# Kernel optimization log

Hardware: AMD Instinct MI355X
Metric: run time of the kernel (lower is better)

Reference implementation:

```python
import jax, jax.numpy as jnp
import numpy as np

N = 100000      # nodes
E = 1600000     # edges
G = 1024        # graphs in batch
NF = 9          # atom features (OGB AtomEncoder)
V = 128         # vocab per atom feature
H = 128         # hidden_dim
L = 3           # num_graph_layers
OUT = 10        # output_dim
BN_EPS = 1e-5


def setup_inputs() -> dict:
    key = jax.random.key(0)
    ks = jax.random.split(key, 12)
    x = jax.random.randint(ks[0], (N, NF), 0, V, dtype=jnp.int32)
    edge_index = jax.random.randint(ks[1], (2, E), 0, N, dtype=jnp.int32)
    batch = jnp.sort(jax.random.randint(ks[2], (N,), 0, G, dtype=jnp.int32))
    emb = jax.random.normal(ks[3], (NF, V, H), dtype=jnp.float32) * 0.05
    Ws = jax.random.normal(ks[4], (L, H, H), dtype=jnp.float32) * (1.0 / np.sqrt(H))
    bs = jnp.zeros((L, H), dtype=jnp.float32)
    gamma = jnp.ones((L - 1, H), dtype=jnp.float32)
    beta = jnp.zeros((L - 1, H), dtype=jnp.float32)
    run_mean = jax.random.normal(ks[5], (L - 1, H), dtype=jnp.float32) * 0.1
    run_var = jax.random.uniform(ks[6], (L - 1, H), minval=0.5, maxval=1.5, dtype=jnp.float32)
    W_clf = jax.random.normal(ks[7], (H, OUT), dtype=jnp.float32) * (1.0 / np.sqrt(H))
    b_clf = jnp.zeros((OUT,), dtype=jnp.float32)
    return {"x": x, "edge_index": edge_index, "batch": batch, "emb": emb,
            "Ws": Ws, "bs": bs, "gamma": gamma, "beta": beta,
            "run_mean": run_mean, "run_var": run_var,
            "W_clf": W_clf, "b_clf": b_clf}


def reference(x, edge_index, batch, emb, Ws, bs, gamma, beta, run_mean, run_var, W_clf, b_clf):
    # Eval-mode forward: dropout = identity, BatchNorm uses running stats.
    src, dst = edge_index[0], edge_index[1]
    # GCN symmetric normalization with self-loops: deg = 1 + in-degree
    deg = jax.ops.segment_sum(jnp.ones((E,), jnp.float32), dst, num_segments=N) + 1.0
    dinv = jax.lax.rsqrt(deg)                 # [N]
    norm_e = dinv[src] * dinv[dst]            # [E] edge coefficient
    norm_self = dinv * dinv                   # [N] self-loop coefficient

    # AtomEncoder: sum of per-feature embedding lookups -> [N, H]
    h = emb[jnp.arange(NF)[None, :], x].sum(axis=1)

    for i in range(L):
        hw = h @ Ws[i]                                                       # [N, H]
        h = (jax.ops.segment_sum(hw[src] * norm_e[:, None], dst, num_segments=N)
             + hw * norm_self[:, None] + bs[i])                              # GCNConv
        if i < L - 1:
            h = (h - run_mean[i]) * (gamma[i] * jax.lax.rsqrt(run_var[i] + BN_EPS)) + beta[i]
            h = jax.nn.relu(h)

    # global mean pool over graphs
    counts = jax.ops.segment_sum(jnp.ones((N,), jnp.float32), batch, num_segments=G)
    pooled = jax.ops.segment_sum(h, batch, num_segments=G) / jnp.maximum(counts, 1.0)[:, None]
    return pooled @ W_clf + b_clf             # [G, OUT]
```

## Files before the change

### kernel.cpp

```cpp
#include <hip/hip_runtime.h>
#include <hip/hip_bf16.h>
#include <hip/hip_fp16.h>

#define NN 100000
#define EE 1600000
#define GG 1024
#define NF 9
#define VV 128
#define HH 128
#define LL 3
#define OUTD 10
#define BN_EPS 1e-5f
#define NBUCK 196
#define BCAP 12288
#define CHUNK 4096
#define NSPLIT 391
#define NENC 3125
#define NB128 782

typedef __attribute__((ext_vector_type(8))) short short8;
typedef __attribute__((ext_vector_type(4))) float f32x4;

__device__ inline unsigned short f2bf(float x) {
    unsigned u = __float_as_uint(x);
    unsigned r = (u + 0x7fffu + ((u >> 16) & 1u)) >> 16;
    return (unsigned short)r;
}
__device__ inline float bf2f(unsigned short b) { return __uint_as_float(((unsigned)b) << 16); }

__device__ inline void mix8(float a[8], const uint4& r, float nm) {
    asm("v_fma_mix_f32 %0, %8, %12, %0 op_sel:[0,0,0] op_sel_hi:[1,0,0]\n\t"
        "v_fma_mix_f32 %1, %8, %12, %1 op_sel:[1,0,0] op_sel_hi:[1,0,0]\n\t"
        "v_fma_mix_f32 %2, %9, %12, %2 op_sel:[0,0,0] op_sel_hi:[1,0,0]\n\t"
        "v_fma_mix_f32 %3, %9, %12, %3 op_sel:[1,0,0] op_sel_hi:[1,0,0]\n\t"
        "v_fma_mix_f32 %4, %10, %12, %4 op_sel:[0,0,0] op_sel_hi:[1,0,0]\n\t"
        "v_fma_mix_f32 %5, %10, %12, %5 op_sel:[1,0,0] op_sel_hi:[1,0,0]\n\t"
        "v_fma_mix_f32 %6, %11, %12, %6 op_sel:[0,0,0] op_sel_hi:[1,0,0]\n\t"
        "v_fma_mix_f32 %7, %11, %12, %7 op_sel:[1,0,0] op_sel_hi:[1,0,0]"
        : "+v"(a[0]), "+v"(a[1]), "+v"(a[2]), "+v"(a[3]),
          "+v"(a[4]), "+v"(a[5]), "+v"(a[6]), "+v"(a[7])
        : "v"(r.x), "v"(r.y), "v"(r.z), "v"(r.w), "v"(nm));
}

__global__ __launch_bounds__(256) void wprep_kernel(const float* __restrict__ Ws,
        const float* __restrict__ Wc, const float* __restrict__ b2,
        unsigned short* __restrict__ WThi, unsigned short* __restrict__ WTlo,
        unsigned short* __restrict__ WcThi, unsigned short* __restrict__ WcTlo,
        float* __restrict__ bb2, int* __restrict__ bcur, float* __restrict__ pooled) {
    int id = blockIdx.x * 256 + threadIdx.x;
    if (id < LL * HH * HH) {
        int layer = id >> 14;
        int rem = id & (HH * HH - 1);
        int k = rem >> 7, n = rem & 127;
        float w = Ws[id];
        unsigned short hi = f2bf(w);
        float lo = w - bf2f(hi);
        WThi[(size_t)layer * HH * HH + n * HH + k] = hi;
        WTlo[(size_t)layer * HH * HH + n * HH + k] = f2bf(lo);
    }
    int tid = threadIdx.x;
    if (blockIdx.x == 0) {
        const float* W2 = Ws + (size_t)2 * HH * HH;
        for (int i = tid; i < 16 * HH; i += 256) {
            int n = i >> 7, k = i & 127;
            float s = 0.f;
            if (n < OUTD) {
                for (int j = 0; j < HH; ++j)
                    s += W2[k * HH + j] * Wc[j * OUTD + n];
            }
            unsigned short hi = f2bf(s);
            WcThi[i] = hi;
            WcTlo[i] = f2bf(s - bf2f(hi));
        }
        if (tid < OUTD) {
            float s = 0.f;
            for (int c = 0; c < HH; ++c) s += b2[c] * Wc[c * OUTD + tid];
            bb2[tid] = s;
        }
    } else if (blockIdx.x == 1) {
        bcur[tid] = 0;
    } else if (blockIdx.x >= 2 && blockIdx.x < 66) {
        pooled[(blockIdx.x - 2) * 256 + tid] = 0.f;
    }
}

__global__ __launch_bounds__(256) void split_enc_kernel(
        const int* __restrict__ src, const int* __restrict__ dst,
        int* __restrict__ bcur, int* __restrict__ bucket_edges,
        const int* __restrict__ x, const float* __restrict__ emb,
        const unsigned short* __restrict__ WThi, const unsigned short* __restrict__ WTlo,
        __half* __restrict__ hw_out) {
    __shared__ __align__(16) char smem_raw[25600];
    int tid = threadIdx.x;
    if (blockIdx.x < NSPLIT) {
        int* lcnt  = (int*)smem_raw;
        int* loff  = lcnt + 256;
        int* lcur  = loff + 256;
        int* gbase = lcur + 256;
        int* sh    = gbase + 256;
        int* stage = sh + 256;
        unsigned char* stageb = (unsigned char*)(stage + CHUNK);
        int cs = blockIdx.x * CHUNK;
        int n = min(CHUNK, EE - cs);
        lcnt[tid] = 0;
        __syncthreads();
        for (int i = tid; i < n; i += 256)
            atomicAdd(&lcnt[dst[cs + i] >> 9], 1);
        __syncthreads();
        int val = lcnt[tid];
        sh[tid] = val; __syncthreads();
        for (int d = 1; d < 256; d <<= 1) {
            int t = (tid >= d) ? sh[tid - d] : 0;
            __syncthreads();
            sh[tid] += t;
            __syncthreads();
        }
        loff[tid] = sh[tid] - val;
        lcur[tid] = sh[tid] - val;
        __syncthreads();
        for (int i = tid; i < n; i += 256) {
            int d = dst[cs + i], s = src[cs + i];
            int b = d >> 9;
            int p = atomicAdd(&lcur[b], 1);
            stage[p] = (s << 9) | (d & 511);
            stageb[p] = (unsigned char)b;
        }
        if (val > 0) gbase[tid] = atomicAdd(&bcur[tid], val);
        __syncthreads();
        for (int i = tid; i < n; i += 256) {
            int b = stageb[i];
            bucket_edges[(size_t)b * BCAP + gbase[b] + (i - loff[b])] = stage[i];
        }
    } else {
        unsigned short (*lh)[136] = (unsigned short(*)[136])smem_raw;
        unsigned short (*ll)[136] = (unsigned short(*)[136])(smem_raw + 32 * 136 * 2);
        int nloc = tid >> 3;
        int seg = tid & 7;
        int nodebase = (blockIdx.x - NSPLIT) * 32;
        int n = nodebase + nloc;
        float s[16];
#pragma unroll
        for (int i = 0; i < 16; ++i) s[i] = 0.f;
#pragma unroll
        for (int f = 0; f < NF; ++f) {
            int idx = x[n * NF + f];
            const float4* ep = (const float4*)(emb + ((size_t)(f * VV + idx)) * HH + seg * 16);
#pragma unroll
            for (int q = 0; q < 4; ++q) {
                float4 e = ep[q];
                s[q * 4 + 0] += e.x; s[q * 4 + 1] += e.y;
                s[q * 4 + 2] += e.z; s[q * 4 + 3] += e.w;
            }
        }
#pragma unroll
        for (int q = 0; q < 4; ++q) {
            ushort4 oh, ol;
            oh.x = f2bf(s[q * 4 + 0]); ol.x = f2bf(s[q * 4 + 0] - bf2f(oh.x));
            oh.y = f2bf(s[q * 4 + 1]); ol.y = f2bf(s[q * 4 + 1] - bf2f(oh.y));
            oh.z = f2bf(s[q * 4 + 2]); ol.z = f2bf(s[q * 4 + 2] - bf2f(oh.z));
            oh.w = f2bf(s[q * 4 + 3]); ol.w = f2bf(s[q * 4 + 3] - bf2f(oh.w));
            *(ushort4*)&lh[nloc][seg * 16 + q * 4] = oh;
            *(ushort4*)&ll[nloc][seg * 16 + q * 4] = ol;
        }
        __syncthreads();
        int wave = tid >> 6, lane = tid & 63;
        int quad = lane >> 4, m = lane & 15;
        f32x4 acc[2][2] = {};
        int kq = quad * 8;
#pragma unroll
        for (int t = 0; t < 4; ++t) {
            int k0 = t * 32 + kq;
            short8 a0h = *(const short8*)&lh[m][k0];
            short8 a0l = *(const short8*)&ll[m][k0];
            short8 a1h = *(const short8*)&lh[16 + m][k0];
            short8 a1l = *(const short8*)&ll[16 + m][k0];
#pragma unroll
            for (int c = 0; c < 2; ++c) {
                int ct = wave * 2 + c;
                short8 bh = *(const short8*)(WThi + (size_t)(ct * 16 + m) * HH + k0);
                short8 bl = *(const short8*)(WTlo + (size_t)(ct * 16 + m) * HH + k0);
                acc[0][c] = __builtin_amdgcn_mfma_f32_16x16x32_bf16(a0h, bh, acc[0][c], 0, 0, 0);
                acc[0][c] = __builtin_amdgcn_mfma_f32_16x16x32_bf16(a0l, bh, acc[0][c], 0, 0, 0);
                acc[0][c] = __builtin_amdgcn_mfma_f32_16x16x32_bf16(a0h, bl, acc[0][c], 0, 0, 0);
                acc[1][c] = __builtin_amdgcn_mfma_f32_16x16x32_bf16(a1h, bh, acc[1][c], 0, 0, 0);
                acc[1][c] = __builtin_amdgcn_mfma_f32_16x16x32_bf16(a1l, bh, acc[1][c], 0, 0, 0);
                acc[1][c] = __builtin_amdgcn_mfma_f32_16x16x32_bf16(a1h, bl, acc[1][c], 0, 0, 0);
            }
        }
#pragma unroll
        for (int c = 0; c < 2; ++c) {
            int colx = (wave * 2 + c) * 16 + m;
#pragma unroll
            for (int rt = 0; rt < 2; ++rt) {
                int r0 = nodebase + rt * 16 + quad * 4;
#pragma unroll
                for (int reg = 0; reg < 4; ++reg)
                    hw_out[(size_t)(r0 + reg) * HH + colx] = __float2half(acc[rt][c][reg]);
            }
        }
    }
}

__global__ __launch_bounds__(256) void bhist_kernel(const int* __restrict__ bcur,
                                                    const int* __restrict__ bucket_edges,
                                                    int* __restrict__ cnt,
                                                    float* __restrict__ dinv,
                                                    int* __restrict__ bsum) {
    __shared__ int lc[512];
    __shared__ int sh[256];
    int b = blockIdx.x, tid = threadIdx.x;
    lc[tid] = 0; lc[tid + 256] = 0;
    __syncthreads();
    int n = bcur[b];
    const int* be = bucket_edges + (size_t)b * BCAP;
    for (int i = tid; i < n; i += 256) atomicAdd(&lc[be[i] & 511], 1);
    __syncthreads();
    int node = b * 512 + tid;
    int c0 = lc[tid], c1 = lc[tid + 256];
    int s = 0;
    if (node < NN) { cnt[node] = c0; dinv[node] = rsqrtf(1.0f + (float)c0); s += c0; }
    if (node + 256 < NN) { cnt[node + 256] = c1; dinv[node + 256] = rsqrtf(1.0f + (float)c1); s += c1; }
    sh[tid] = s; __syncthreads();
    for (int d = 128; d > 0; d >>= 1) { if (tid < d) sh[tid] += sh[tid + d]; __syncthreads(); }
    if (tid == 0) bsum[b] = sh[0];
}

__global__ void scanC_kernel(const int* __restrict__ cnt, const int* __restrict__ bsum,
                             int* __restrict__ row_ptr) {
    __shared__ int sh[256];
    __shared__ int pre[256];
    int tid = threadIdx.x;
    pre[tid] = (tid < blockIdx.x && tid < NBUCK) ? bsum[tid] : 0;
    __syncthreads();
    for (int d = 128; d > 0; d >>= 1) { if (tid < d) pre[tid] += pre[tid + d]; __syncthreads(); }
    int bbase = pre[0];
    int base = blockIdx.x * 512 + tid * 2;
    int v0 = (base < NN) ? cnt[base] : 0;
    int v1 = (base + 1 < NN) ? cnt[base + 1] : 0;
    int ts = v0 + v1;
    sh[tid] = ts; __syncthreads();
    for (int d = 1; d < 256; d <<= 1) {
        int t = (tid >= d) ? sh[tid - d] : 0;
        __syncthreads();
        sh[tid] += t;
        __syncthreads();
    }
    int excl = sh[tid] - ts + bbase;
    if (base < NN) row_ptr[base] = excl;
    if (base + 1 < NN) row_ptr[base + 1] = excl + v0;
    if (blockIdx.x == 0 && tid == 0) row_ptr[NN] = EE;
}

__global__ __launch_bounds__(256) void cscatter_kernel(const int* __restrict__ bcur,
                                                       const int* __restrict__ bucket_edges,
                                                       const int* __restrict__ row_ptr,
                                                       const float* __restrict__ dinv,
                                                       int2* __restrict__ col) {
    __shared__ int lcur[512];
    int b = blockIdx.x, tid = threadIdx.x;
    int node0 = b * 512;
#pragma unroll
    for (int k = 0; k < 2; ++k) {
        int j = tid + k * 256;
        int node = node0 + j;
        if (node < NN) lcur[j] = row_ptr[node];
    }
    __syncthreads();
    int n = bcur[b];
    const int* be = bucket_edges + (size_t)b * BCAP;
    for (int i = tid; i < n; i += 256) {
        int w = be[i];
        int j = w & 511;
        int s = (int)((unsigned)w >> 9);
        int p = atomicAdd(&lcur[j], 1);
        float nm = dinv[s] * dinv[node0 + j];
        col[p] = make_int2(s, __float_as_int(nm));
    }
}

__device__ inline void gather_node(const uint4* __restrict__ hw4,
                                   const int2* __restrict__ col,
                                   int start, int end, int c4,
                                   float a[8], float b[8]) {
    int e = start;
    for (; e + 4 <= end; e += 4) {
        unsigned long long w0 = *(const unsigned long long*)&col[e];
        unsigned long long w1 = *(const unsigned long long*)&col[e + 1];
        unsigned long long w2 = *(const unsigned long long*)&col[e + 2];
        unsigned long long w3 = *(const unsigned long long*)&col[e + 3];
        uint4 r0 = hw4[(size_t)(unsigned)(w0 & 0xffffffffu) * 16 + c4];
        uint4 r1 = hw4[(size_t)(unsigned)(w1 & 0xffffffffu) * 16 + c4];
        uint4 r2 = hw4[(size_t)(unsigned)(w2 & 0xffffffffu) * 16 + c4];
        uint4 r3 = hw4[(size_t)(unsigned)(w3 & 0xffffffffu) * 16 + c4];
        mix8(a, r0, __int_as_float((int)(unsigned)(w0 >> 32)));
        mix8(b, r1, __int_as_float((int)(unsigned)(w1 >> 32)));
        mix8(a, r2, __int_as_float((int)(unsigned)(w2 >> 32)));
        mix8(b, r3, __int_as_float((int)(unsigned)(w3 >> 32)));
    }
    if (e < end) {
        int last = end - 1;
        int e1 = min(e + 1, last), e2 = min(e + 2, last), e3 = min(e + 3, last);
        unsigned long long w0 = *(const unsigned long long*)&col[e];
        unsigned long long w1 = *(const unsigned long long*)&col[e1];
        unsigned long long w2 = *(const unsigned long long*)&col[e2];
        unsigned long long w3 = *(const unsigned long long*)&col[e3];
        float n0 = __int_as_float((int)(unsigned)(w0 >> 32));
        float n1 = (e + 1 < end) ? __int_as_float((int)(unsigned)(w1 >> 32)) : 0.f;
        float n2 = (e + 2 < end) ? __int_as_float((int)(unsigned)(w2 >> 32)) : 0.f;
        float n3 = (e + 3 < end) ? __int_as_float((int)(unsigned)(w3 >> 32)) : 0.f;
        uint4 r0 = hw4[(size_t)(unsigned)(w0 & 0xffffffffu) * 16 + c4];
        uint4 r1 = hw4[(size_t)(unsigned)(w1 & 0xffffffffu) * 16 + c4];
        uint4 r2 = hw4[(size_t)(unsigned)(w2 & 0xffffffffu) * 16 + c4];
        uint4 r3 = hw4[(size_t)(unsigned)(w3 & 0xffffffffu) * 16 + c4];
        mix8(a, r0, n0);
        mix8(b, r1, n1);
        mix8(a, r2, n2);
        mix8(b, r3, n3);
    }
}

template<bool DO_PROJ>
__global__ __launch_bounds__(512) void agg_mm_kernel(const __half* __restrict__ hw_in,
    const int* __restrict__ row_ptr, const int2* __restrict__ col,
    const float* __restrict__ dinv,
    const float* __restrict__ bias, const float* __restrict__ gamma,
    const float* __restrict__ beta, const float* __restrict__ rmean,
    const float* __restrict__ rvar,
    const unsigned short* __restrict__ WThi, const unsigned short* __restrict__ WTlo,
    __half* __restrict__ hw_out,
    const unsigned short* __restrict__ WcThi, const unsigned short* __restrict__ WcTlo,
    __half* __restrict__ y_out) {
    __shared__ __align__(16) unsigned short lh[32][136];
    __shared__ __align__(16) unsigned short ll[32][136];
    int wave = threadIdx.x >> 6;
    int lane = threadIdx.x & 63;
    int grp = lane >> 4;
    int c4 = lane & 15;
    int nodebase = blockIdx.x * 32;
    const uint4* hw4 = (const uint4*)hw_in;

    int v = nodebase + wave * 4 + grp;
    int start = row_ptr[v], end = row_ptr[v + 1];
    float a[8] = {}, b[8] = {};
    gather_node(hw4, col, start, end, c4, a, b);

    {
        float dv = dinv[v];
        uint4 r = hw4[(size_t)v * 16 + c4];
        mix8(a, r, dv * dv);
    }
#pragma unroll
    for (int i = 0; i < 8; ++i) a[i] += b[i];

    int ch = c4 * 8;
#pragma unroll
    for (int i = 0; i < 8; ++i) a[i] += bias[ch + i];
#pragma unroll
    for (int i = 0; i < 8; ++i) {
        int c = ch + i;
        float sc = gamma[c] * rsqrtf(rvar[c] + BN_EPS);
        a[i] = fmaxf((a[i] - rmean[c]) * sc + beta[c], 0.f);
    }
    int rloc = wave * 4 + grp;
    ushort4 oh0, oh1, ol0, ol1;
    oh0.x = f2bf(a[0]); ol0.x = f2bf(a[0] - bf2f(oh0.x));
    oh0.y = f2bf(a[1]); ol0.y = f2bf(a[1] - bf2f(oh0.y));
    oh0.z = f2bf(a[2]); ol0.z = f2bf(a[2] - bf2f(oh0.z));
    oh0.w = f2bf(a[3]); ol0.w = f2bf(a[3] - bf2f(oh0.w));
    oh1.x = f2bf(a[4]); ol1.x = f2bf(a[4] - bf2f(oh1.x));
    oh1.y = f2bf(a[5]); ol1.y = f2bf(a[5] - bf2f(oh1.y));
    oh1.z = f2bf(a[6]); ol1.z = f2bf(a[6] - bf2f(oh1.z));
    oh1.w = f2bf(a[7]); ol1.w = f2bf(a[7] - bf2f(oh1.w));
    *(ushort4*)&lh[rloc][ch]     = oh0;
    *(ushort4*)&lh[rloc][ch + 4] = oh1;
    *(ushort4*)&ll[rloc][ch]     = ol0;
    *(ushort4*)&ll[rloc][ch + 4] = ol1;

    __syncthreads();
    int quad = lane >> 4, m = lane & 15;
    f32x4 acc[2] = {};
    int kq = quad * 8;
    int ct = wave;
#pragma unroll
    for (int t = 0; t < 4; ++t) {
        int k0 = t * 32 + kq;
        short8 a0h = *(const short8*)&lh[m][k0];
        short8 a0l = *(const short8*)&ll[m][k0];
        short8 a1h = *(const short8*)&lh[16 + m][k0];
        short8 a1l = *(const short8*)&ll[16 + m][k0];
        short8 bh = *(const short8*)(WThi + (size_t)(ct * 16 + m) * HH + k0);
        short8 bl = *(const short8*)(WTlo + (size_t)(ct * 16 + m) * HH + k0);
        acc[0] = __builtin_amdgcn_mfma_f32_16x16x32_bf16(a0h, bh, acc[0], 0, 0, 0);
        acc[0] = __builtin_amdgcn_mfma_f32_16x16x32_bf16(a0l, bh, acc[0], 0, 0, 0);
        acc[0] = __builtin_amdgcn_mfma_f32_16x16x32_bf16(a0h, bl, acc[0], 0, 0, 0);
        acc[1] = __builtin_amdgcn_mfma_f32_16x16x32_bf16(a1h, bh, acc[1], 0, 0, 0);
        acc[1] = __builtin_amdgcn_mfma_f32_16x16x32_bf16(a1l, bh, acc[1], 0, 0, 0);
        acc[1] = __builtin_amdgcn_mfma_f32_16x16x32_bf16(a1h, bl, acc[1], 0, 0, 0);
    }
    int colx = ct * 16 + m;
#pragma unroll
    for (int rt = 0; rt < 2; ++rt) {
        int r0 = nodebase + rt * 16 + quad * 4;
#pragma unroll
        for (int reg = 0; reg < 4; ++reg)
            hw_out[(size_t)(r0 + reg) * HH + colx] = __float2half(acc[rt][reg]);
    }

    if constexpr (DO_PROJ) {
        if (wave < 2) {
            f32x4 pacc = {};
#pragma unroll
            for (int t = 0; t < 4; ++t) {
                int k0 = t * 32 + kq;
                short8 ah = *(const short8*)&lh[wave * 16 + m][k0];
                short8 al = *(const short8*)&ll[wave * 16 + m][k0];
                short8 bh = *(const short8*)(WcThi + (size_t)m * HH + k0);
                short8 bl = *(const short8*)(WcTlo + (size_t)m * HH + k0);
                pacc = __builtin_amdgcn_mfma_f32_16x16x32_bf16(ah, bh, pacc, 0, 0, 0);
                pacc = __builtin_amdgcn_mfma_f32_16x16x32_bf16(al, bh, pacc, 0, 0, 0);
                pacc = __builtin_amdgcn_mfma_f32_16x16x32_bf16(ah, bl, pacc, 0, 0, 0);
            }
#pragma unroll
            for (int reg = 0; reg < 4; ++reg) {
                int node = nodebase + wave * 16 + quad * 4 + reg;
                y_out[(size_t)node * 16 + m] = __float2half(pacc[reg]);
            }
        }
    }
}

__global__ __launch_bounds__(256) void agg_pool_kernel(const __half* __restrict__ y,
    const int* __restrict__ row_ptr, const int2* __restrict__ col,
    const float* __restrict__ dinv, const int* __restrict__ batch,
    float* __restrict__ pooled) {
    __shared__ __align__(16) float lz[128][16];
    __shared__ int bg[128];
    int tid = threadIdx.x;
    int g2 = tid >> 1;
    int cl = tid & 1;
    int nodebase = blockIdx.x * 128;
    int v = nodebase + g2;
    int vc = min(v, NN - 1);
    int start = row_ptr[vc];
    int end = (v < NN) ? row_ptr[vc + 1] : start;
    const uint4* y4 = (const uint4*)y;
    float a[8] = {};
    int e = start;
    for (; e + 4 <= end; e += 4) {
        unsigned long long w0 = *(const unsigned long long*)&col[e];
        unsigned long long w1 = *(const unsigned long long*)&col[e + 1];
        unsigned long long w2 = *(const unsigned long long*)&col[e + 2];
        unsigned long long w3 = *(const unsigned long long*)&col[e + 3];
        uint4 r0 = y4[(size_t)(unsigned)(w0 & 0xffffffffu) * 2 + cl];
        uint4 r1 = y4[(size_t)(unsigned)(w1 & 0xffffffffu) * 2 + cl];
        uint4 r2 = y4[(size_t)(unsigned)(w2 & 0xffffffffu) * 2 + cl];
        uint4 r3 = y4[(size_t)(unsigned)(w3 & 0xffffffffu) * 2 + cl];
        mix8(a, r0, __int_as_float((int)(unsigned)(w0 >> 32)));
        mix8(a, r1, __int_as_float((int)(unsigned)(w1 >> 32)));
        mix8(a, r2, __int_as_float((int)(unsigned)(w2 >> 32)));
        mix8(a, r3, __int_as_float((int)(unsigned)(w3 >> 32)));
    }
    if (e < end) {
        int last = end - 1;
        int e1 = min(e + 1, last), e2 = min(e + 2, last), e3 = min(e + 3, last);
        unsigned long long w0 = *(const unsigned long long*)&col[e];
        unsigned long long w1 = *(const unsigned long long*)&col[e1];
        unsigned long long w2 = *(const unsigned long long*)&col[e2];
        unsigned long long w3 = *(const unsigned long long*)&col[e3];
        float n0 = __int_as_float((int)(unsigned)(w0 >> 32));
        float n1 = (e + 1 < end) ? __int_as_float((int)(unsigned)(w1 >> 32)) : 0.f;
        float n2 = (e + 2 < end) ? __int_as_float((int)(unsigned)(w2 >> 32)) : 0.f;
        float n3 = (e + 3 < end) ? __int_as_float((int)(unsigned)(w3 >> 32)) : 0.f;
        uint4 r0 = y4[(size_t)(unsigned)(w0 & 0xffffffffu) * 2 + cl];
        uint4 r1 = y4[(size_t)(unsigned)(w1 & 0xffffffffu) * 2 + cl];
        uint4 r2 = y4[(size_t)(unsigned)(w2 & 0xffffffffu) * 2 + cl];
        uint4 r3 = y4[(size_t)(unsigned)(w3 & 0xffffffffu) * 2 + cl];
        mix8(a, r0, n0);
        mix8(a, r1, n1);
        mix8(a, r2, n2);
        mix8(a, r3, n3);
    }
    if (v < NN) {
        float dv = dinv[v];
        uint4 r = y4[(size_t)v * 2 + cl];
        mix8(a, r, dv * dv);
    } else {
#pragma unroll
        for (int i = 0; i < 8; ++i) a[i] = 0.f;
    }
    int chb = cl * 8;
#pragma unroll
    for (int i = 0; i < 8; ++i) lz[g2][chb + i] = a[i];
    if (cl == 0) bg[g2] = batch[vc];
    __syncthreads();
    int ch = tid & 15;
    int rh = tid >> 4;
    int r0i = rh * 8;
    int curg = bg[r0i];
    float run = 0.f;
    for (int r = r0i; r < r0i + 8; ++r) {
        int gg = bg[r];
        if (gg != curg) {
            atomicAdd(&pooled[(size_t)curg * 16 + ch], run);
            run = 0.f; curg = gg;
        }
        run += lz[r][ch];
    }
    atomicAdd(&pooled[(size_t)curg * 16 + ch], run);
}

__global__ __launch_bounds__(256) void finalize_kernel(const float* __restrict__ pooled,
    const int* __restrict__ batch, const float* __restrict__ bb2,
    const float* __restrict__ bc, float* __restrict__ out) {
    int id = blockIdx.x * 256 + threadIdx.x;
    if (id >= GG * 16) return;
    int g = id >> 4, o = id & 15;
    if (o >= OUTD) return;
    int lo = 0, hi = NN;
    while (lo < hi) { int mid = (lo + hi) >> 1; if (batch[mid] < g) lo = mid + 1; else hi = mid; }
    int s0 = lo;
    lo = 0; hi = NN;
    int g1 = g + 1;
    while (lo < hi) { int mid = (lo + hi) >> 1; if (batch[mid] < g1) lo = mid + 1; else hi = mid; }
    int cnt = lo - s0;
    float r = pooled[(size_t)g * 16 + o] / fmaxf((float)cnt, 1.0f);
    out[(size_t)g * OUTD + o] = r + ((cnt > 0) ? bb2[o] : 0.f) + bc[o];
}

extern "C" void kernel_launch(void* const* d_in, const int* in_sizes, int n_in,
                              void* d_out, int out_size, void* d_ws, size_t ws_size,
                              hipStream_t stream) {
    const int*   x      = (const int*)d_in[0];
    const int*   eidx   = (const int*)d_in[1];
    const int*   batch  = (const int*)d_in[2];
    const float* emb    = (const float*)d_in[3];
    const float* Ws     = (const float*)d_in[4];
    const float* bs     = (const float*)d_in[5];
    const float* gamma  = (const float*)d_in[6];
    const float* beta   = (const float*)d_in[7];
    const float* rmean  = (const float*)d_in[8];
    const float* rvar   = (const float*)d_in[9];
    const float* Wclf   = (const float*)d_in[10];
    const float* bclf   = (const float*)d_in[11];
    float* out = (float*)d_out;

    const int* e_src = eidx;
    const int* e_dst = eidx + EE;

    char* ws = (char*)d_ws;
    size_t off = 0;
    auto take = [&](size_t bytes) -> void* {
        void* p = ws + off;
        off = (off + bytes + 255) & ~(size_t)255;
        return p;
    };
    float* dinv     = (float*)take((size_t)NN * 4);
    int*   cnt      = (int*)  take((size_t)NN * 4);
    int*   row_ptr  = (int*)  take((size_t)(NN + 1) * 4);
    int*   bsum     = (int*)  take((size_t)NBUCK * 4);
    int*   bcur     = (int*)  take((size_t)256 * 4);
    int*   bucket_edges = (int*)take((size_t)NBUCK * BCAP * 4);
    int2*  col      = (int2*) take((size_t)EE * 8 + 64);
    __half* hwA     = (__half*)take((size_t)NN * HH * 2);
    __half* hwB     = (__half*)take((size_t)NN * HH * 2);
    __half* yh      = (__half*)take((size_t)NN * 16 * 2);
    float* pooled   = (float*)take((size_t)GG * 16 * 4);
    unsigned short* WThi = (unsigned short*)take((size_t)LL * HH * HH * 2);
    unsigned short* WTlo = (unsigned short*)take((size_t)LL * HH * HH * 2);
    unsigned short* WcThi = (unsigned short*)take((size_t)16 * HH * 2);
    unsigned short* WcTlo = (unsigned short*)take((size_t)16 * HH * 2);
    float* bb2      = (float*)take((size_t)16 * 4);

    wprep_kernel<<<(LL * HH * HH + 255) / 256, 256, 0, stream>>>(Ws, Wclf, bs + 2 * HH,
        WThi, WTlo, WcThi, WcTlo, bb2, bcur, pooled);
    split_enc_kernel<<<NSPLIT + NENC, 256, 0, stream>>>(e_src, e_dst, bcur, bucket_edges,
        x, emb, WThi, WTlo, hwA);
    bhist_kernel<<<NBUCK, 256, 0, stream>>>(bcur, bucket_edges, cnt, dinv, bsum);
    scanC_kernel<<<NBUCK, 256, 0, stream>>>(cnt, bsum, row_ptr);
    cscatter_kernel<<<NBUCK, 256, 0, stream>>>(bcur, bucket_edges, row_ptr, dinv, col);

    agg_mm_kernel<false><<<NN / 32, 512, 0, stream>>>(hwA, row_ptr, col, dinv,
        bs, gamma, beta, rmean, rvar,
        WThi + (size_t)1 * HH * HH, WTlo + (size_t)1 * HH * HH, hwB,
        nullptr, nullptr, nullptr);
    agg_mm_kernel<true><<<NN / 32, 512, 0, stream>>>(hwB, row_ptr, col, dinv,
        bs + HH, gamma + HH, beta + HH, rmean + HH, rvar + HH,
        WThi + (size_t)2 * HH * HH, WTlo + (size_t)2 * HH * HH, hwA,
        WcThi, WcTlo, yh);
    agg_pool_kernel<<<NB128, 256, 0, stream>>>(yh, row_ptr, col, dinv, batch, pooled);
    finalize_kernel<<<(GG * 16 + 255) / 256, 256, 0, stream>>>(pooled, batch, bb2, bclf, out);
}
```

Measured before the change: 394.7 us.

## Spread encoder blocks across CSR-build kernels and skip dead layer-3 matmul

The 3125 encoder+first-matmul blocks are split into four groups (1100/900/300/825) and appended to the split, histogram, scan and scatter kernels. The small 196-block CSR-build kernels then have extra independent work to fill the GPU. Separately, the last aggregation kernel no longer computes or writes the unused layer-3 hw matmul output; it only computes the classifier projection. The risk is that the encoder blocks lengthen each of the short serial kernels, and the larger shared-memory footprint may affect their occupancy.

```diff
diff --git a/kernel.cpp b/kernel.cpp
--- a/kernel.cpp
+++ b/kernel.cpp
@@ -17,6 +17,10 @@
 #define NSPLIT 391
 #define NENC 3125
 #define NB128 782
+#define EN1 1100
+#define EN2 900
+#define EN3 300
+#define EN4 825
 
 typedef __attribute__((ext_vector_type(8))) short short8;
 typedef __attribute__((ext_vector_type(4))) float f32x4;
@@ -40,6 +44,231 @@
         : "+v"(a[0]), "+v"(a[1]), "+v"(a[2]), "+v"(a[3]),
           "+v"(a[4]), "+v"(a[5]), "+v"(a[6]), "+v"(a[7])
         : "v"(r.x), "v"(r.y), "v"(r.z), "v"(r.w), "v"(nm));
+}
+
+
+__device__ void enc_body(char* smem_raw, int tid, int encblk,
+        const int* __restrict__ x, const float* __restrict__ emb,
+        const unsigned short* __restrict__ WThi, const unsigned short* __restrict__ WTlo,
+        __half* __restrict__ hw_out) {
+    unsigned short (*lh)[136] = (unsigned short(*)[136])smem_raw;
+    unsigned short (*ll)[136] = (unsigned short(*)[136])(smem_raw + 32 * 136 * 2);
+    int nloc = tid >> 3;
+    int seg = tid & 7;
+    int nodebase = encblk * 32;
+    int n = nodebase + nloc;
+    float s[16];
+#pragma unroll
+    for (int i = 0; i < 16; ++i) s[i] = 0.f;
+#pragma unroll
+    for (int f = 0; f < NF; ++f) {
+        int idx = x[n * NF + f];
+        const float4* ep = (const float4*)(emb + ((size_t)(f * VV + idx)) * HH + seg * 16);
+#pragma unroll
+        for (int q = 0; q < 4; ++q) {
+            float4 e = ep[q];
+            s[q * 4 + 0] += e.x; s[q * 4 + 1] += e.y;
+            s[q * 4 + 2] += e.z; s[q * 4 + 3] += e.w;
+        }
+    }
+#pragma unroll
+    for (int q = 0; q < 4; ++q) {
+        ushort4 oh, ol;
+        oh.x = f2bf(s[q * 4 + 0]); ol.x = f2bf(s[q * 4 + 0] - bf2f(oh.x));
+        oh.y = f2bf(s[q * 4 + 1]); ol.y = f2bf(s[q * 4 + 1] - bf2f(oh.y));
+        oh.z = f2bf(s[q * 4 + 2]); ol.z = f2bf(s[q * 4 + 2] - bf2f(oh.z));
+        oh.w = f2bf(s[q * 4 + 3]); ol.w = f2bf(s[q * 4 + 3] - bf2f(oh.w));
+        *(ushort4*)&lh[nloc][seg * 16 + q * 4] = oh;
+        *(ushort4*)&ll[nloc][seg * 16 + q * 4] = ol;
+    }
+    __syncthreads();
+    int wave = tid >> 6, lane = tid & 63;
+    int quad = lane >> 4, m = lane & 15;
+    f32x4 acc[2][2] = {};
+    int kq = quad * 8;
+#pragma unroll
+    for (int t = 0; t < 4; ++t) {
+        int k0 = t * 32 + kq;
+        short8 a0h = *(const short8*)&lh[m][k0];
+        short8 a0l = *(const short8*)&ll[m][k0];
+        short8 a1h = *(const short8*)&lh[16 + m][k0];
+        short8 a1l = *(const short8*)&ll[16 + m][k0];
+#pragma unroll
+        for (int c = 0; c < 2; ++c) {
+            int ct = wave * 2 + c;
+            short8 bh = *(const short8*)(WThi + (size_t)(ct * 16 + m) * HH + k0);
+            short8 bl = *(const short8*)(WTlo + (size_t)(ct * 16 + m) * HH + k0);
+            acc[0][c] = __builtin_amdgcn_mfma_f32_16x16x32_bf16(a0h, bh, acc[0][c], 0, 0, 0);
+            acc[0][c] = __builtin_amdgcn_mfma_f32_16x16x32_bf16(a0l, bh, acc[0][c], 0, 0, 0);
+            acc[0][c] = __builtin_amdgcn_mfma_f32_16x16x32_bf16(a0h, bl, acc[0][c], 0, 0, 0);
+            acc[1][c] = __builtin_amdgcn_mfma_f32_16x16x32_bf16(a1h, bh, acc[1][c], 0, 0, 0);
+            acc[1][c] = __builtin_amdgcn_mfma_f32_16x16x32_bf16(a1l, bh, acc[1][c], 0, 0, 0);
+            acc[1][c] = __builtin_amdgcn_mfma_f32_16x16x32_bf16(a1h, bl, acc[1][c], 0, 0, 0);
+        }
+    }
+#pragma unroll
+    for (int c = 0; c < 2; ++c) {
+        int colx = (wave * 2 + c) * 16 + m;
+#pragma unroll
+        for (int rt = 0; rt < 2; ++rt) {
+            int r0 = nodebase + rt * 16 + quad * 4;
+#pragma unroll
+            for (int reg = 0; reg < 4; ++reg)
+                hw_out[(size_t)(r0 + reg) * HH + colx] = __float2half(acc[rt][c][reg]);
+        }
+    }
+}
+
+
+__global__ __launch_bounds__(256) void split_enc_kernel(
+        const int* __restrict__ src, const int* __restrict__ dst,
+        int* __restrict__ bcur, int* __restrict__ bucket_edges,
+        const int* __restrict__ x, const float* __restrict__ emb,
+        const unsigned short* __restrict__ WThi, const unsigned short* __restrict__ WTlo,
+        __half* __restrict__ hw_out) {
+    __shared__ __align__(16) char smem_raw[25600];
+    int tid = threadIdx.x;
+    if (blockIdx.x >= NSPLIT) {
+        enc_body(smem_raw, tid, blockIdx.x - NSPLIT, x, emb, WThi, WTlo, hw_out);
+        return;
+    }
+    int* lcnt  = (int*)smem_raw;
+    int* loff  = lcnt + 256;
+    int* lcur  = loff + 256;
+    int* gbase = lcur + 256;
+    int* sh    = gbase + 256;
+    int* stage = sh + 256;
+    unsigned char* stageb = (unsigned char*)(stage + CHUNK);
+    int cs = blockIdx.x * CHUNK;
+    int n = min(CHUNK, EE - cs);
+    lcnt[tid] = 0;
+    __syncthreads();
+    for (int i = tid; i < n; i += 256)
+        atomicAdd(&lcnt[dst[cs + i] >> 9], 1);
+    __syncthreads();
+    int val = lcnt[tid];
+    sh[tid] = val; __syncthreads();
+    for (int d = 1; d < 256; d <<= 1) {
+        int t = (tid >= d) ? sh[tid - d] : 0;
+        __syncthreads();
+        sh[tid] += t;
+        __syncthreads();
+    }
+    loff[tid] = sh[tid] - val;
+    lcur[tid] = sh[tid] - val;
+    __syncthreads();
+    for (int i = tid; i < n; i += 256) {
+        int d = dst[cs + i], s = src[cs + i];
+        int b = d >> 9;
+        int p = atomicAdd(&lcur[b], 1);
+        stage[p] = (s << 9) | (d & 511);
+        stageb[p] = (unsigned char)b;
+    }
+    if (val > 0) gbase[tid] = atomicAdd(&bcur[tid], val);
+    __syncthreads();
+    for (int i = tid; i < n; i += 256) {
+        int b = stageb[i];
+        bucket_edges[(size_t)b * BCAP + gbase[b] + (i - loff[b])] = stage[i];
+    }
+}
+
+__global__ __launch_bounds__(256) void bhist_enc_kernel(const int* __restrict__ bcur,
+        const int* __restrict__ bucket_edges,
+        int* __restrict__ cnt, float* __restrict__ dinv, int* __restrict__ bsum,
+        const int* __restrict__ x, const float* __restrict__ emb,
+        const unsigned short* __restrict__ WThi, const unsigned short* __restrict__ WTlo,
+        __half* __restrict__ hw_out) {
+    __shared__ __align__(16) char smem_raw[17408];
+    int tid = threadIdx.x;
+    if (blockIdx.x >= NBUCK) {
+        enc_body(smem_raw, tid, EN1 + (blockIdx.x - NBUCK), x, emb, WThi, WTlo, hw_out);
+        return;
+    }
+    int* lc = (int*)smem_raw;
+    int* sh = lc + 512;
+    int b = blockIdx.x;
+    lc[tid] = 0; lc[tid + 256] = 0;
+    __syncthreads();
+    int n = bcur[b];
+    const int* be = bucket_edges + (size_t)b * BCAP;
+    for (int i = tid; i < n; i += 256) atomicAdd(&lc[be[i] & 511], 1);
+    __syncthreads();
+    int node = b * 512 + tid;
+    int c0 = lc[tid], c1 = lc[tid + 256];
+    int s = 0;
+    if (node < NN) { cnt[node] = c0; dinv[node] = rsqrtf(1.0f + (float)c0); s += c0; }
+    if (node + 256 < NN) { cnt[node + 256] = c1; dinv[node + 256] = rsqrtf(1.0f + (float)c1); s += c1; }
+    sh[tid] = s; __syncthreads();
+    for (int d = 128; d > 0; d >>= 1) { if (tid < d) sh[tid] += sh[tid + d]; __syncthreads(); }
+    if (tid == 0) bsum[b] = sh[0];
+}
+
+__global__ __launch_bounds__(256) void scanC_enc_kernel(const int* __restrict__ cnt,
+        const int* __restrict__ bsum, int* __restrict__ row_ptr,
+        const int* __restrict__ x, const float* __restrict__ emb,
+        const unsigned short* __restrict__ WThi, const unsigned short* __restrict__ WTlo,
+        __half* __restrict__ hw_out) {
+    __shared__ __align__(16) char smem_raw[17408];
+    int tid = threadIdx.x;
+    if (blockIdx.x >= NBUCK) {
+        enc_body(smem_raw, tid, EN1 + EN2 + (blockIdx.x - NBUCK), x, emb, WThi, WTlo, hw_out);
+        return;
+    }
+    int* sh  = (int*)smem_raw;
+    int* pre = sh + 256;
+    pre[tid] = (tid < blockIdx.x && tid < NBUCK) ? bsum[tid] : 0;
+    __syncthreads();
+    for (int d = 128; d > 0; d >>= 1) { if (tid < d) pre[tid] += pre[tid + d]; __syncthreads(); }
+    int bbase = pre[0];
+    int base = blockIdx.x * 512 + tid * 2;
+    int v0 = (base < NN) ? cnt[base] : 0;
+    int v1 = (base + 1 < NN) ? cnt[base + 1] : 0;
+    int ts = v0 + v1;
+    sh[tid] = ts; __syncthreads();
+    for (int d = 1; d < 256; d <<= 1) {
+        int t = (tid >= d) ? sh[tid - d] : 0;
+        __syncthreads();
+        sh[tid] += t;
+        __syncthreads();
+    }
+    int excl = sh[tid] - ts + bbase;
+    if (base < NN) row_ptr[base] = excl;
+    if (base + 1 < NN) row_ptr[base + 1] = excl + v0;
+    if (blockIdx.x == 0 && tid == 0) row_ptr[NN] = EE;
+}
+
+__global__ __launch_bounds__(256) void cscatter_enc_kernel(const int* __restrict__ bcur,
+        const int* __restrict__ bucket_edges, const int* __restrict__ row_ptr,
+        const float* __restrict__ dinv, int2* __restrict__ col,
+        const int* __restrict__ x, const float* __restrict__ emb,
+        const unsigned short* __restrict__ WThi, const unsigned short* __restrict__ WTlo,
+        __half* __restrict__ hw_out) {
+    __shared__ __align__(16) char smem_raw[17408];
+    int tid = threadIdx.x;
+    if (blockIdx.x >= NBUCK) {
+        enc_body(smem_raw, tid, EN1 + EN2 + EN3 + (blockIdx.x - NBUCK), x, emb, WThi, WTlo, hw_out);
+        return;
+    }
+    int* lcur = (int*)smem_raw;
+    int b = blockIdx.x;
+    int node0 = b * 512;
+#pragma unroll
+    for (int k = 0; k < 2; ++k) {
+        int j = tid + k * 256;
+        int node = node0 + j;
+        if (node < NN) lcur[j] = row_ptr[node];
+    }
+    __syncthreads();
+    int n = bcur[b];
+    const int* be = bucket_edges + (size_t)b * BCAP;
+    for (int i = tid; i < n; i += 256) {
+        int w = be[i];
+        int j = w & 511;
+        int s = (int)((unsigned)w >> 9);
+        int p = atomicAdd(&lcur[j], 1);
+        float nm = dinv[s] * dinv[node0 + j];
+        col[p] = make_int2(s, __float_as_int(nm));
+    }
 }
 
 __global__ __launch_bounds__(256) void wprep_kernel(const float* __restrict__ Ws,
@@ -81,200 +310,6 @@
         bcur[tid] = 0;
     } else if (blockIdx.x >= 2 && blockIdx.x < 66) {
         pooled[(blockIdx.x - 2) * 256 + tid] = 0.f;
-    }
-}
-
-__global__ __launch_bounds__(256) void split_enc_kernel(
-        const int* __restrict__ src, const int* __restrict__ dst,
-        int* __restrict__ bcur, int* __restrict__ bucket_edges,
-        const int* __restrict__ x, const float* __restrict__ emb,
-        const unsigned short* __restrict__ WThi, const unsigned short* __restrict__ WTlo,
-        __half* __restrict__ hw_out) {
-    __shared__ __align__(16) char smem_raw[25600];
-    int tid = threadIdx.x;
-    if (blockIdx.x < NSPLIT) {
-        int* lcnt  = (int*)smem_raw;
-        int* loff  = lcnt + 256;
-        int* lcur  = loff + 256;
-        int* gbase = lcur + 256;
-        int* sh    = gbase + 256;
-        int* stage = sh + 256;
-        unsigned char* stageb = (unsigned char*)(stage + CHUNK);
-        int cs = blockIdx.x * CHUNK;
-        int n = min(CHUNK, EE - cs);
-        lcnt[tid] = 0;
-        __syncthreads();
-        for (int i = tid; i < n; i += 256)
-            atomicAdd(&lcnt[dst[cs + i] >> 9], 1);
-        __syncthreads();
-        int val = lcnt[tid];
-        sh[tid] = val; __syncthreads();
-        for (int d = 1; d < 256; d <<= 1) {
-            int t = (tid >= d) ? sh[tid - d] : 0;
-            __syncthreads();
-            sh[tid] += t;
-            __syncthreads();
-        }
-        loff[tid] = sh[tid] - val;
-        lcur[tid] = sh[tid] - val;
-        __syncthreads();
-        for (int i = tid; i < n; i += 256) {
-            int d = dst[cs + i], s = src[cs + i];
-            int b = d >> 9;
-            int p = atomicAdd(&lcur[b], 1);
-            stage[p] = (s << 9) | (d & 511);
-            stageb[p] = (unsigned char)b;
-        }
-        if (val > 0) gbase[tid] = atomicAdd(&bcur[tid], val);
-        __syncthreads();
-        for (int i = tid; i < n; i += 256) {
-            int b = stageb[i];
-            bucket_edges[(size_t)b * BCAP + gbase[b] + (i - loff[b])] = stage[i];
-        }
-    } else {
-        unsigned short (*lh)[136] = (unsigned short(*)[136])smem_raw;
-        unsigned short (*ll)[136] = (unsigned short(*)[136])(smem_raw + 32 * 136 * 2);
-        int nloc = tid >> 3;
-        int seg = tid & 7;
-        int nodebase = (blockIdx.x - NSPLIT) * 32;
-        int n = nodebase + nloc;
-        float s[16];
-#pragma unroll
-        for (int i = 0; i < 16; ++i) s[i] = 0.f;
-#pragma unroll
-        for (int f = 0; f < NF; ++f) {
-            int idx = x[n * NF + f];
-            const float4* ep = (const float4*)(emb + ((size_t)(f * VV + idx)) * HH + seg * 16);
-#pragma unroll
-            for (int q = 0; q < 4; ++q) {
-                float4 e = ep[q];
-                s[q * 4 + 0] += e.x; s[q * 4 + 1] += e.y;
-                s[q * 4 + 2] += e.z; s[q * 4 + 3] += e.w;
-            }
-        }
-#pragma unroll
-        for (int q = 0; q < 4; ++q) {
-            ushort4 oh, ol;
-            oh.x = f2bf(s[q * 4 + 0]); ol.x = f2bf(s[q * 4 + 0] - bf2f(oh.x));
-            oh.y = f2bf(s[q * 4 + 1]); ol.y = f2bf(s[q * 4 + 1] - bf2f(oh.y));
-            oh.z = f2bf(s[q * 4 + 2]); ol.z = f2bf(s[q * 4 + 2] - bf2f(oh.z));
-            oh.w = f2bf(s[q * 4 + 3]); ol.w = f2bf(s[q * 4 + 3] - bf2f(oh.w));
-            *(ushort4*)&lh[nloc][seg * 16 + q * 4] = oh;
-            *(ushort4*)&ll[nloc][seg * 16 + q * 4] = ol;
-        }
-        __syncthreads();
-        int wave = tid >> 6, lane = tid & 63;
-        int quad = lane >> 4, m = lane & 15;
-        f32x4 acc[2][2] = {};
-        int kq = quad * 8;
-#pragma unroll
-        for (int t = 0; t < 4; ++t) {
-            int k0 = t * 32 + kq;
-            short8 a0h = *(const short8*)&lh[m][k0];
-            short8 a0l = *(const short8*)&ll[m][k0];
-            short8 a1h = *(const short8*)&lh[16 + m][k0];
-            short8 a1l = *(const short8*)&ll[16 + m][k0];
-#pragma unroll
-            for (int c = 0; c < 2; ++c) {
-                int ct = wave * 2 + c;
-                short8 bh = *(const short8*)(WThi + (size_t)(ct * 16 + m) * HH + k0);
-                short8 bl = *(const short8*)(WTlo + (size_t)(ct * 16 + m) * HH + k0);
-                acc[0][c] = __builtin_amdgcn_mfma_f32_16x16x32_bf16(a0h, bh, acc[0][c], 0, 0, 0);
-                acc[0][c] = __builtin_amdgcn_mfma_f32_16x16x32_bf16(a0l, bh, acc[0][c], 0, 0, 0);
-                acc[0][c] = __builtin_amdgcn_mfma_f32_16x16x32_bf16(a0h, bl, acc[0][c], 0, 0, 0);
-                acc[1][c] = __builtin_amdgcn_mfma_f32_16x16x32_bf16(a1h, bh, acc[1][c], 0, 0, 0);
-                acc[1][c] = __builtin_amdgcn_mfma_f32_16x16x32_bf16(a1l, bh, acc[1][c], 0, 0, 0);
-                acc[1][c] = __builtin_amdgcn_mfma_f32_16x16x32_bf16(a1h, bl, acc[1][c], 0, 0, 0);
-            }
-        }
-#pragma unroll
-        for (int c = 0; c < 2; ++c) {
-            int colx = (wave * 2 + c) * 16 + m;
-#pragma unroll
-            for (int rt = 0; rt < 2; ++rt) {
-                int r0 = nodebase + rt * 16 + quad * 4;
-#pragma unroll
-                for (int reg = 0; reg < 4; ++reg)
-                    hw_out[(size_t)(r0 + reg) * HH + colx] = __float2half(acc[rt][c][reg]);
-            }
-        }
-    }
-}
-
-__global__ __launch_bounds__(256) void bhist_kernel(const int* __restrict__ bcur,
-                                                    const int* __restrict__ bucket_edges,
-                                                    int* __restrict__ cnt,
-                                                    float* __restrict__ dinv,
-                                                    int* __restrict__ bsum) {
-    __shared__ int lc[512];
-    __shared__ int sh[256];
-    int b = blockIdx.x, tid = threadIdx.x;
-    lc[tid] = 0; lc[tid + 256] = 0;
-    __syncthreads();
-    int n = bcur[b];
-    const int* be = bucket_edges + (size_t)b * BCAP;
-    for (int i = tid; i < n; i += 256) atomicAdd(&lc[be[i] & 511], 1);
-    __syncthreads();
-    int node = b * 512 + tid;
-    int c0 = lc[tid], c1 = lc[tid + 256];
-    int s = 0;
-    if (node < NN) { cnt[node] = c0; dinv[node] = rsqrtf(1.0f + (float)c0); s += c0; }
-    if (node + 256 < NN) { cnt[node + 256] = c1; dinv[node + 256] = rsqrtf(1.0f + (float)c1); s += c1; }
-    sh[tid] = s; __syncthreads();
-    for (int d = 128; d > 0; d >>= 1) { if (tid < d) sh[tid] += sh[tid + d]; __syncthreads(); }
-    if (tid == 0) bsum[b] = sh[0];
-}
-
-__global__ void scanC_kernel(const int* __restrict__ cnt, const int* __restrict__ bsum,
-                             int* __restrict__ row_ptr) {
-    __shared__ int sh[256];
-    __shared__ int pre[256];
-    int tid = threadIdx.x;
-    pre[tid] = (tid < blockIdx.x && tid < NBUCK) ? bsum[tid] : 0;
-    __syncthreads();
-    for (int d = 128; d > 0; d >>= 1) { if (tid < d) pre[tid] += pre[tid + d]; __syncthreads(); }
-    int bbase = pre[0];
-    int base = blockIdx.x * 512 + tid * 2;
-    int v0 = (base < NN) ? cnt[base] : 0;
-    int v1 = (base + 1 < NN) ? cnt[base + 1] : 0;
-    int ts = v0 + v1;
-    sh[tid] = ts; __syncthreads();
-    for (int d = 1; d < 256; d <<= 1) {
-        int t = (tid >= d) ? sh[tid - d] : 0;
-        __syncthreads();
-        sh[tid] += t;
-        __syncthreads();
-    }
-    int excl = sh[tid] - ts + bbase;
-    if (base < NN) row_ptr[base] = excl;
-    if (base + 1 < NN) row_ptr[base + 1] = excl + v0;
-    if (blockIdx.x == 0 && tid == 0) row_ptr[NN] = EE;
-}
-
-__global__ __launch_bounds__(256) void cscatter_kernel(const int* __restrict__ bcur,
-                                                       const int* __restrict__ bucket_edges,
-                                                       const int* __restrict__ row_ptr,
-                                                       const float* __restrict__ dinv,
-                                                       int2* __restrict__ col) {
-    __shared__ int lcur[512];
-    int b = blockIdx.x, tid = threadIdx.x;
-    int node0 = b * 512;
-#pragma unroll
-    for (int k = 0; k < 2; ++k) {
-        int j = tid + k * 256;
-        int node = node0 + j;
-        if (node < NN) lcur[j] = row_ptr[node];
-    }
-    __syncthreads();
-    int n = bcur[b];
-    const int* be = bucket_edges + (size_t)b * BCAP;
-    for (int i = tid; i < n; i += 256) {
-        int w = be[i];
-        int j = w & 511;
-        int s = (int)((unsigned)w >> 9);
-        int p = atomicAdd(&lcur[j], 1);
-        float nm = dinv[s] * dinv[node0 + j];
-        col[p] = make_int2(s, __float_as_int(nm));
     }
 }
 
@@ -378,35 +413,35 @@
 
     __syncthreads();
     int quad = lane >> 4, m = lane & 15;
-    f32x4 acc[2] = {};
     int kq = quad * 8;
-    int ct = wave;
-#pragma unroll
-    for (int t = 0; t < 4; ++t) {
-        int k0 = t * 32 + kq;
-        short8 a0h = *(const short8*)&lh[m][k0];
-        short8 a0l = *(const short8*)&ll[m][k0];
-        short8 a1h = *(const short8*)&lh[16 + m][k0];
-        short8 a1l = *(const short8*)&ll[16 + m][k0];
-        short8 bh = *(const short8*)(WThi + (size_t)(ct * 16 + m) * HH + k0);
-        short8 bl = *(const short8*)(WTlo + (size_t)(ct * 16 + m) * HH + k0);
-        acc[0] = __builtin_amdgcn_mfma_f32_16x16x32_bf16(a0h, bh, acc[0], 0, 0, 0);
-        acc[0] = __builtin_amdgcn_mfma_f32_16x16x32_bf16(a0l, bh, acc[0], 0, 0, 0);
-        acc[0] = __builtin_amdgcn_mfma_f32_16x16x32_bf16(a0h, bl, acc[0], 0, 0, 0);
-        acc[1] = __builtin_amdgcn_mfma_f32_16x16x32_bf16(a1h, bh, acc[1], 0, 0, 0);
-        acc[1] = __builtin_amdgcn_mfma_f32_16x16x32_bf16(a1l, bh, acc[1], 0, 0, 0);
-        acc[1] = __builtin_amdgcn_mfma_f32_16x16x32_bf16(a1h, bl, acc[1], 0, 0, 0);
-    }
-    int colx = ct * 16 + m;
-#pragma unroll
-    for (int rt = 0; rt < 2; ++rt) {
-        int r0 = nodebase + rt * 16 + quad * 4;
-#pragma unroll
-        for (int reg = 0; reg < 4; ++reg)
-            hw_out[(size_t)(r0 + reg) * HH + colx] = __float2half(acc[rt][reg]);
-    }
-
-    if constexpr (DO_PROJ) {
+    if constexpr (!DO_PROJ) {
+        f32x4 acc[2] = {};
+        int ct = wave;
+#pragma unroll
+        for (int t = 0; t < 4; ++t) {
+            int k0 = t * 32 + kq;
+            short8 a0h = *(const short8*)&lh[m][k0];
+            short8 a0l = *(const short8*)&ll[m][k0];
+            short8 a1h = *(const short8*)&lh[16 + m][k0];
+            short8 a1l = *(const short8*)&ll[16 + m][k0];
+            short8 bh = *(const short8*)(WThi + (size_t)(ct * 16 + m) * HH + k0);
+            short8 bl = *(const short8*)(WTlo + (size_t)(ct * 16 + m) * HH + k0);
+            acc[0] = __builtin_amdgcn_mfma_f32_16x16x32_bf16(a0h, bh, acc[0], 0, 0, 0);
+            acc[0] = __builtin_amdgcn_mfma_f32_16x16x32_bf16(a0l, bh, acc[0], 0, 0, 0);
+            acc[0] = __builtin_amdgcn_mfma_f32_16x16x32_bf16(a0h, bl, acc[0], 0, 0, 0);
+            acc[1] = __builtin_amdgcn_mfma_f32_16x16x32_bf16(a1h, bh, acc[1], 0, 0, 0);
+            acc[1] = __builtin_amdgcn_mfma_f32_16x16x32_bf16(a1l, bh, acc[1], 0, 0, 0);
+            acc[1] = __builtin_amdgcn_mfma_f32_16x16x32_bf16(a1h, bl, acc[1], 0, 0, 0);
+        }
+        int colx = ct * 16 + m;
+#pragma unroll
+        for (int rt = 0; rt < 2; ++rt) {
+            int r0 = nodebase + rt * 16 + quad * 4;
+#pragma unroll
+            for (int reg = 0; reg < 4; ++reg)
+                hw_out[(size_t)(r0 + reg) * HH + colx] = __float2half(acc[rt][reg]);
+        }
+    } else {
         if (wave < 2) {
             f32x4 pacc = {};
 #pragma unroll
@@ -573,11 +608,14 @@
 
     wprep_kernel<<<(LL * HH * HH + 255) / 256, 256, 0, stream>>>(Ws, Wclf, bs + 2 * HH,
         WThi, WTlo, WcThi, WcTlo, bb2, bcur, pooled);
-    split_enc_kernel<<<NSPLIT + NENC, 256, 0, stream>>>(e_src, e_dst, bcur, bucket_edges,
+    split_enc_kernel<<<NSPLIT + EN1, 256, 0, stream>>>(e_src, e_dst, bcur, bucket_edges,
         x, emb, WThi, WTlo, hwA);
-    bhist_kernel<<<NBUCK, 256, 0, stream>>>(bcur, bucket_edges, cnt, dinv, bsum);
-    scanC_kernel<<<NBUCK, 256, 0, stream>>>(cnt, bsum, row_ptr);
-    cscatter_kernel<<<NBUCK, 256, 0, stream>>>(bcur, bucket_edges, row_ptr, dinv, col);
+    bhist_enc_kernel<<<NBUCK + EN2, 256, 0, stream>>>(bcur, bucket_edges, cnt, dinv, bsum,
+        x, emb, WThi, WTlo, hwA);
+    scanC_enc_kernel<<<NBUCK + EN3, 256, 0, stream>>>(cnt, bsum, row_ptr,
+        x, emb, WThi, WTlo, hwA);
+    cscatter_enc_kernel<<<NBUCK + EN4, 256, 0, stream>>>(bcur, bucket_edges, row_ptr, dinv, col,
+        x, emb, WThi, WTlo, hwA);
 
     agg_mm_kernel<false><<<NN / 32, 512, 0, stream>>>(hwA, row_ptr, col, dinv,
         bs, gamma, beta, rmean, rvar,
@@ -585,7 +623,7 @@
         nullptr, nullptr, nullptr);
     agg_mm_kernel<true><<<NN / 32, 512, 0, stream>>>(hwB, row_ptr, col, dinv,
         bs + HH, gamma + HH, beta + HH, rmean + HH, rvar + HH,
-        WThi + (size_t)2 * HH * HH, WTlo + (size_t)2 * HH * HH, hwA,
+        nullptr, nullptr, nullptr,
         WcThi, WcTlo, yh);
     agg_pool_kernel<<<NB128, 256, 0, stream>>>(yh, row_ptr, col, dinv, batch, pooled);
     finalize_kernel<<<(GG * 16 + 255) / 256, 256, 0, stream>>>(pooled, batch, bb2, bclf, out);
```

Measured after the change: 380.1 us. 3.7% less time.
